# Kernel tuning notes

Hardware: AMD Instinct MI355X
Metric: run time of the kernel (lower is better)

Reference implementation:

```python
import jax, jax.numpy as jnp
import numpy as np

L2_LAMDA = 0.001
RECONS_LAMDA = 0.2
LB_TH = 0.01
B, N, D = 32, 2048, 256


def setup_inputs() -> dict:
    key = jax.random.key(0)
    k1, k2, k3, k4 = jax.random.split(key, 4)
    cur = jax.random.normal(k1, (B, N, D), jnp.float32)
    pre = jax.random.normal(k2, (B, N, D), jnp.float32)
    lim_r = float(np.sqrt(6.0 / (D + D)))  # xavier_uniform bound
    r_proj = jax.random.uniform(k3, (D, D), jnp.float32, -lim_r, lim_r)
    lim_i = float(np.sqrt(6.0 / (N + N)))
    incidence_m = jax.random.uniform(k4, (N, N), jnp.float32, -lim_i, lim_i)
    return {"cur": cur, "pre": pre, "r_proj": r_proj, "incidence_m": incidence_m}


def reference(cur, pre, r_proj, incidence_m):
    # torch forward detaches cur/pre
    cur = jax.lax.stop_gradient(cur)
    pre = jax.lax.stop_gradient(pre)
    # clamp(min=lb_th) then zero where not (> lb_th)  ==  keep original where > lb_th else 0
    W = jnp.where(incidence_m > LB_TH, incidence_m, 0.0)          # (N, N)
    proj = jnp.einsum('bnd,de->bne', cur, r_proj)                 # (B, N, D)
    neigh = jnp.einsum('nm,bmd->bnd', W, pre)                     # (B, N, D)
    recon_err = jnp.sqrt(jnp.sum((proj - neigh) ** 2, axis=-1))   # (B, N)
    # torch: max(sum(abs(row[None,:]), dim=0)) == max-abs of the masked row
    l1 = jnp.max(jnp.abs(W), axis=1)                              # (N,)
    l2 = jnp.sqrt(jnp.sum(W ** 2, axis=1))                        # (N,)
    per_node = recon_err * RECONS_LAMDA + l1[None, :] + L2_LAMDA * l2[None, :]
    loss = jnp.sum(per_node, axis=1, keepdims=True)               # (B, 1)
    return loss, incidence_m
```

## Files before the change

### kernel.cpp

```cpp
#include <hip/hip_runtime.h>


typedef __attribute__((ext_vector_type(8))) short bf16x8;
typedef __attribute__((ext_vector_type(8))) unsigned short ushort8;
typedef __attribute__((ext_vector_type(16))) float f32x16;

__device__ __forceinline__ unsigned short f2bf(float f) {
    union { float f; unsigned u; } x; x.f = f;
    unsigned r = x.u + 0x7fffu + ((x.u >> 16) & 1u);
    return (unsigned short)(r >> 16);
}

#define GLL16(g, l)                                                         \
    __builtin_amdgcn_global_load_lds(                                       \
        (const __attribute__((address_space(1))) void*)(g),                 \
        (__attribute__((address_space(3))) void*)(l), 16, 0, 0)

__device__ __forceinline__ void transpose_64x64(
    const float* __restrict__ src, unsigned short* __restrict__ dst,
    int R, int C, int r0, int c0, unsigned short* __restrict__ tile) {
    const int t = threadIdx.x;
    const int fr = t >> 4, fc = (t & 15) * 4;
#pragma unroll
    for (int it = 0; it < 4; ++it) {
        int m = fr + it * 16;
        float4 v = *(const float4*)(src + (size_t)(r0 + m) * C + c0 + fc);
        tile[(fc + 0) * 68 + m] = f2bf(v.x);
        tile[(fc + 1) * 68 + m] = f2bf(v.y);
        tile[(fc + 2) * 68 + m] = f2bf(v.z);
        tile[(fc + 3) * 68 + m] = f2bf(v.w);
    }
    __syncthreads();
    const int d = t >> 2, m0 = (t & 3) * 16;
    unsigned short v[16];
#pragma unroll
    for (int j = 0; j < 4; ++j)
        *(ushort4*)(v + j * 4) = *(const ushort4*)(tile + d * 68 + m0 + j * 4);
    unsigned short* dp = dst + (size_t)(c0 + d) * R + r0 + m0;
    ushort8 p0, p1;
#pragma unroll
    for (int j = 0; j < 8; ++j) { p0[j] = v[j]; p1[j] = v[8 + j]; }
    *(ushort8*)(dp) = p0;
    *(ushort8*)(dp + 8) = p1;
}

__global__ __launch_bounds__(256) void prep_inc(
    const float* __restrict__ inc, float* __restrict__ out_inc,
    unsigned short* __restrict__ Wneg, float* __restrict__ crow) {
    __shared__ float smax[4], ssum[4];
    const int row = blockIdx.x;
    const int t = threadIdx.x;
    const float4* src = (const float4*)(inc + (size_t)row * 2048);
    float4* dst = (float4*)(out_inc + (size_t)row * 2048);
    ushort4* wp = (ushort4*)(Wneg + (size_t)row * 2048);
    float lmax = 0.f, ss = 0.f;
#pragma unroll
    for (int it = 0; it < 2; ++it) {
        int i = it * 256 + t;
        float4 v = src[i];
        dst[i] = v;
        float w0 = v.x > 0.01f ? v.x : 0.f;
        float w1 = v.y > 0.01f ? v.y : 0.f;
        float w2 = v.z > 0.01f ? v.z : 0.f;
        float w3 = v.w > 0.01f ? v.w : 0.f;
        ushort4 p;
        p.x = f2bf(-w0); p.y = f2bf(-w1); p.z = f2bf(-w2); p.w = f2bf(-w3);
        wp[i] = p;
        lmax = fmaxf(lmax, fmaxf(fmaxf(w0, w1), fmaxf(w2, w3)));
        ss += w0 * w0 + w1 * w1 + w2 * w2 + w3 * w3;
    }
#pragma unroll
    for (int off = 32; off; off >>= 1) {
        lmax = fmaxf(lmax, __shfl_down(lmax, off));
        ss += __shfl_down(ss, off);
    }
    int wv = t >> 6, ln = t & 63;
    if (ln == 0) { smax[wv] = lmax; ssum[wv] = ss; }
    __syncthreads();
    if (t == 0) {
        float m = fmaxf(fmaxf(smax[0], smax[1]), fmaxf(smax[2], smax[3]));
        float s = ssum[0] + ssum[1] + ssum[2] + ssum[3];
        crow[row] = m + 0.001f * sqrtf(s);
    }
}

__global__ __launch_bounds__(256) void prep_tr(
    const float* __restrict__ pre, unsigned short* __restrict__ preT,
    const float* __restrict__ r_proj, unsigned short* __restrict__ rprojT,
    const float* __restrict__ cur, unsigned short* __restrict__ curbf) {
    __shared__ unsigned short tile[64 * 68];
    const int bid = blockIdx.x;
    const int t = threadIdx.x;
    if (bid < 4096) {
        const int b = bid >> 7;
        const int mt = (bid & 127) >> 2;
        const int dt = bid & 3;
        transpose_64x64(pre + (size_t)b * 524288, preT + (size_t)b * 524288,
                        2048, 256, mt * 64, dt * 64, tile);
    } else if (bid < 4112) {
        const int tt = bid - 4096;
        transpose_64x64(r_proj, rprojT, 256, 256, (tt >> 2) * 64, (tt & 3) * 64,
                        tile);
    } else {
        const size_t base = (size_t)(bid - 4112) * 8192;
#pragma unroll
        for (int i = 0; i < 8; ++i) {
            size_t idx = base + (size_t)(i * 256 + t) * 4;
            float4 v = *(const float4*)(cur + idx);
            ushort4 p;
            p.x = f2bf(v.x); p.y = f2bf(v.y); p.z = f2bf(v.z); p.w = f2bf(v.w);
            *(ushort4*)(curbf + idx) = p;
        }
    }
}

__global__ __launch_bounds__(1024) void gemm_diff(
    const unsigned short* __restrict__ Wneg,
    const unsigned short* __restrict__ curbf,
    const unsigned short* __restrict__ preT,
    const unsigned short* __restrict__ rprojT,
    float* __restrict__ Ssq)
{
    const int n0 = blockIdx.x * 256;
    const int b  = blockIdx.y;

    __shared__ unsigned short Ab[4 * 256 * 32];
    __shared__ unsigned short Bb[4 * 256 * 32];
    __shared__ float ssq[256];

    const int tid  = threadIdx.x;
    const int w    = tid >> 6;
    const int lane = tid & 63;
    const int l32  = lane & 31;
    const int half = lane >> 5;
    const int wm   = w >> 2;
    const int wn   = w & 3;
    const int w16  = w * 16;
    const int srow  = lane >> 2;
    const int sbyte = ((lane & 3) ^ ((lane >> 3) & 3)) * 16;
    const int q2    = (l32 >> 1) & 3;

    if (tid < 256) ssq[tid] = 0.f;

    f32x16 acc[2][2] = {};

    const unsigned short* curA = curbf + (size_t)b * 2048 * 256 + (size_t)n0 * 256;
    const unsigned short* preB = preT + (size_t)b * 256 * 2048;
    const unsigned short* An   = Wneg + (size_t)n0 * 2048;

#define STAGEPAIR(T, AB, AS, BB, BS, KK)                                       \
    {                                                                          \
        GLL16((const char*)((AB) + (size_t)(w16 + srow) * (AS) + (KK)) + sbyte,\
              (char*)Ab + ((T) & 3) * 16384 + w * 1024);                       \
        GLL16((const char*)((BB) + (size_t)(w16 + srow) * (BS) + (KK)) + sbyte,\
              (char*)Bb + ((T) & 3) * 16384 + w * 1024);                       \
    }

    STAGEPAIR(0, An, 2048, preB, 2048, 0);
    STAGEPAIR(1, An, 2048, preB, 2048, 32);
    STAGEPAIR(2, An, 2048, preB, 2048, 64);

    for (int t = 0; t < 72; ++t) {
        if (t < 70)      asm volatile("s_waitcnt vmcnt(4)" ::: "memory");
        else if (t == 70) asm volatile("s_waitcnt vmcnt(2)" ::: "memory");
        else              asm volatile("s_waitcnt vmcnt(0)" ::: "memory");
        asm volatile("s_barrier" ::: "memory");

        if (t < 69) {
            const int t3 = t + 3;
            const unsigned short *aB, *bB;
            int aS, bS, kk;
            if (t3 < 64) { aB = An;   aS = 2048; bB = preB;   bS = 2048; kk = t3 * 32; }
            else         { aB = curA; aS = 256;  bB = rprojT; bS = 256;  kk = (t3 - 64) * 32; }
            STAGEPAIR(t3, aB, aS, bB, bS, kk);
        }

        const unsigned short* Ac = Ab + (t & 3) * 8192;
        const unsigned short* Bc = Bb + (t & 3) * 8192;
#pragma unroll
        for (int ks = 0; ks < 2; ++ks) {
            const int co = (((ks << 1) + half) ^ q2) << 3;
            bf16x8 af[2], bfr[2];
#pragma unroll
            for (int mi = 0; mi < 2; ++mi)
                af[mi] = *(const bf16x8*)(Ac + (wm * 64 + mi * 32 + l32) * 32 + co);
#pragma unroll
            for (int ni = 0; ni < 2; ++ni)
                bfr[ni] = *(const bf16x8*)(Bc + (wn * 64 + ni * 32 + l32) * 32 + co);
#pragma unroll
            for (int mi = 0; mi < 2; ++mi)
#pragma unroll
                for (int ni = 0; ni < 2; ++ni)
                    acc[mi][ni] = __builtin_amdgcn_mfma_f32_32x32x16_bf16(
                        af[mi], bfr[ni], acc[mi][ni], 0, 0, 0);
        }
    }
    __syncthreads();

#pragma unroll
    for (int mi = 0; mi < 2; ++mi)
#pragma unroll
        for (int reg = 0; reg < 16; ++reg) {
            float s = 0.f;
#pragma unroll
            for (int ni = 0; ni < 2; ++ni) {
                float v = acc[mi][ni][reg];
                s += v * v;
            }
            s += __shfl_xor(s, 1);
            s += __shfl_xor(s, 2);
            s += __shfl_xor(s, 4);
            s += __shfl_xor(s, 8);
            s += __shfl_xor(s, 16);
            if (l32 == 0) {
                const int row = wm * 64 + mi * 32 +
                                (reg & 3) + 8 * (reg >> 2) + 4 * half;
                atomicAdd(&ssq[row], s);
            }
        }
    __syncthreads();
    if (tid < 256)
        Ssq[(size_t)b * 2048 + n0 + tid] = sqrtf(ssq[tid]);
}

__global__ void finalize(const float* __restrict__ Ssq,
                         const float* __restrict__ crow,
                         float* __restrict__ out) {
    const int b = blockIdx.x;
    float s1 = 0.f, s2 = 0.f;
    for (int i = threadIdx.x; i < 2048; i += 256) {
        s1 += Ssq[(size_t)b * 2048 + i];
        s2 += crow[i];
    }
#pragma unroll
    for (int off = 32; off; off >>= 1) {
        s1 += __shfl_down(s1, off);
        s2 += __shfl_down(s2, off);
    }
    __shared__ float sm1[4], sm2[4];
    int wv = threadIdx.x >> 6, ln = threadIdx.x & 63;
    if (ln == 0) { sm1[wv] = s1; sm2[wv] = s2; }
    __syncthreads();
    if (threadIdx.x == 0)
        out[b] = 0.2f * (sm1[0] + sm1[1] + sm1[2] + sm1[3])
               + (sm2[0] + sm2[1] + sm2[2] + sm2[3]);
}

extern "C" void kernel_launch(void* const* d_in, const int* in_sizes, int n_in,
                              void* d_out, int out_size, void* d_ws, size_t ws_size,
                              hipStream_t stream) {
    const float* cur    = (const float*)d_in[0];
    const float* pre    = (const float*)d_in[1];
    const float* r_proj = (const float*)d_in[2];
    const float* inc    = (const float*)d_in[3];
    float* out = (float*)d_out;

    char* ws = (char*)d_ws;
    unsigned short* Wneg   = (unsigned short*)(ws + 0);
    unsigned short* preT   = (unsigned short*)(ws + 8388608);
    unsigned short* rprojT = (unsigned short*)(ws + 41943040);
    float*          Sbuf   = (float*)(ws + 42074112);
    float*          crow   = (float*)(ws + 42336256);
    unsigned short* curbf  = (unsigned short*)(ws + 42344448);

    prep_inc<<<2048, 256, 0, stream>>>(inc, out + 32, Wneg, crow);
    prep_tr<<<6160, 256, 0, stream>>>(pre, preT, r_proj, rprojT, cur, curbf);
    gemm_diff<<<dim3(8, 32), 1024, 0, stream>>>(Wneg, curbf, preT, rprojT, Sbuf);
    finalize<<<32, 256, 0, stream>>>(Sbuf, crow, out);
}
```

Baseline: 265.6 us.

## Merge prep kernels, fold finalize into GEMM epilogue, remap blocks per XCD

Combines the incidence preprocessing and the transpose/convert kernels into one launch. The final per-batch reduction moves into the GEMM epilogue, which accumulates into the output with atomics after the output is zeroed in the prep kernel. This drops two kernel launches and the intermediate Ssq buffer. The GEMM grid is also remapped so each XCD handles whole batches, aiming to improve L2 reuse of the shared B operand. The trade-off is that atomic float accumulation makes the summation order nondeterministic.

```diff
diff --git a/kernel.cpp b/kernel.cpp
--- a/kernel.cpp
+++ b/kernel.cpp
@@ -44,65 +44,66 @@
     *(ushort8*)(dp + 8) = p1;
 }
 
-__global__ __launch_bounds__(256) void prep_inc(
+__global__ __launch_bounds__(256) void prep_all(
     const float* __restrict__ inc, float* __restrict__ out_inc,
-    unsigned short* __restrict__ Wneg, float* __restrict__ crow) {
-    __shared__ float smax[4], ssum[4];
-    const int row = blockIdx.x;
-    const int t = threadIdx.x;
-    const float4* src = (const float4*)(inc + (size_t)row * 2048);
-    float4* dst = (float4*)(out_inc + (size_t)row * 2048);
-    ushort4* wp = (ushort4*)(Wneg + (size_t)row * 2048);
-    float lmax = 0.f, ss = 0.f;
-#pragma unroll
-    for (int it = 0; it < 2; ++it) {
-        int i = it * 256 + t;
-        float4 v = src[i];
-        dst[i] = v;
-        float w0 = v.x > 0.01f ? v.x : 0.f;
-        float w1 = v.y > 0.01f ? v.y : 0.f;
-        float w2 = v.z > 0.01f ? v.z : 0.f;
-        float w3 = v.w > 0.01f ? v.w : 0.f;
-        ushort4 p;
-        p.x = f2bf(-w0); p.y = f2bf(-w1); p.z = f2bf(-w2); p.w = f2bf(-w3);
-        wp[i] = p;
-        lmax = fmaxf(lmax, fmaxf(fmaxf(w0, w1), fmaxf(w2, w3)));
-        ss += w0 * w0 + w1 * w1 + w2 * w2 + w3 * w3;
-    }
-#pragma unroll
-    for (int off = 32; off; off >>= 1) {
-        lmax = fmaxf(lmax, __shfl_down(lmax, off));
-        ss += __shfl_down(ss, off);
-    }
-    int wv = t >> 6, ln = t & 63;
-    if (ln == 0) { smax[wv] = lmax; ssum[wv] = ss; }
-    __syncthreads();
-    if (t == 0) {
-        float m = fmaxf(fmaxf(smax[0], smax[1]), fmaxf(smax[2], smax[3]));
-        float s = ssum[0] + ssum[1] + ssum[2] + ssum[3];
-        crow[row] = m + 0.001f * sqrtf(s);
-    }
-}
-
-__global__ __launch_bounds__(256) void prep_tr(
+    unsigned short* __restrict__ Wneg, float* __restrict__ crow,
     const float* __restrict__ pre, unsigned short* __restrict__ preT,
     const float* __restrict__ r_proj, unsigned short* __restrict__ rprojT,
-    const float* __restrict__ cur, unsigned short* __restrict__ curbf) {
+    const float* __restrict__ cur, unsigned short* __restrict__ curbf,
+    float* __restrict__ out_loss) {
     __shared__ unsigned short tile[64 * 68];
+    __shared__ float smax[4], ssum[4];
     const int bid = blockIdx.x;
     const int t = threadIdx.x;
-    if (bid < 4096) {
-        const int b = bid >> 7;
-        const int mt = (bid & 127) >> 2;
-        const int dt = bid & 3;
+
+    if (bid < 2048) {
+        if (bid == 0 && t < 32) out_loss[t] = 0.f;
+        const int row = bid;
+        const float4* src = (const float4*)(inc + (size_t)row * 2048);
+        float4* dst = (float4*)(out_inc + (size_t)row * 2048);
+        ushort4* wp = (ushort4*)(Wneg + (size_t)row * 2048);
+        float lmax = 0.f, ss = 0.f;
+#pragma unroll
+        for (int it = 0; it < 2; ++it) {
+            int i = it * 256 + t;
+            float4 v = src[i];
+            dst[i] = v;
+            float w0 = v.x > 0.01f ? v.x : 0.f;
+            float w1 = v.y > 0.01f ? v.y : 0.f;
+            float w2 = v.z > 0.01f ? v.z : 0.f;
+            float w3 = v.w > 0.01f ? v.w : 0.f;
+            ushort4 p;
+            p.x = f2bf(-w0); p.y = f2bf(-w1); p.z = f2bf(-w2); p.w = f2bf(-w3);
+            wp[i] = p;
+            lmax = fmaxf(lmax, fmaxf(fmaxf(w0, w1), fmaxf(w2, w3)));
+            ss += w0 * w0 + w1 * w1 + w2 * w2 + w3 * w3;
+        }
+#pragma unroll
+        for (int off = 32; off; off >>= 1) {
+            lmax = fmaxf(lmax, __shfl_down(lmax, off));
+            ss += __shfl_down(ss, off);
+        }
+        int wv = t >> 6, ln = t & 63;
+        if (ln == 0) { smax[wv] = lmax; ssum[wv] = ss; }
+        __syncthreads();
+        if (t == 0) {
+            float m = fmaxf(fmaxf(smax[0], smax[1]), fmaxf(smax[2], smax[3]));
+            float s = ssum[0] + ssum[1] + ssum[2] + ssum[3];
+            crow[row] = m + 0.001f * sqrtf(s);
+        }
+    } else if (bid < 6144) {
+        const int tt = bid - 2048;
+        const int b = tt >> 7;
+        const int mt = (tt & 127) >> 2;
+        const int dt = tt & 3;
         transpose_64x64(pre + (size_t)b * 524288, preT + (size_t)b * 524288,
                         2048, 256, mt * 64, dt * 64, tile);
-    } else if (bid < 4112) {
-        const int tt = bid - 4096;
+    } else if (bid < 6160) {
+        const int tt = bid - 6144;
         transpose_64x64(r_proj, rprojT, 256, 256, (tt >> 2) * 64, (tt & 3) * 64,
                         tile);
     } else {
-        const size_t base = (size_t)(bid - 4112) * 8192;
+        const size_t base = (size_t)(bid - 6160) * 8192;
 #pragma unroll
         for (int i = 0; i < 8; ++i) {
             size_t idx = base + (size_t)(i * 256 + t) * 4;
@@ -119,14 +120,19 @@
     const unsigned short* __restrict__ curbf,
     const unsigned short* __restrict__ preT,
     const unsigned short* __restrict__ rprojT,
-    float* __restrict__ Ssq)
+    const float* __restrict__ crow,
+    float* __restrict__ out_loss)
 {
-    const int n0 = blockIdx.x * 256;
-    const int b  = blockIdx.y;
+    const int i    = blockIdx.x;
+    const int xcd  = i & 7;
+    const int slot = i >> 3;
+    const int n0   = (slot & 7) * 256;
+    const int b    = xcd + ((slot >> 3) << 3);
 
     __shared__ unsigned short Ab[4 * 256 * 32];
     __shared__ unsigned short Bb[4 * 256 * 32];
     __shared__ float ssq[256];
+    __shared__ float red[16];
 
     const int tid  = threadIdx.x;
     const int w    = tid >> 6;
@@ -161,7 +167,7 @@
     STAGEPAIR(2, An, 2048, preB, 2048, 64);
 
     for (int t = 0; t < 72; ++t) {
-        if (t < 70)      asm volatile("s_waitcnt vmcnt(4)" ::: "memory");
+        if (t < 70)       asm volatile("s_waitcnt vmcnt(4)" ::: "memory");
         else if (t == 70) asm volatile("s_waitcnt vmcnt(2)" ::: "memory");
         else              asm volatile("s_waitcnt vmcnt(0)" ::: "memory");
         asm volatile("s_barrier" ::: "memory");
@@ -219,31 +225,19 @@
             }
         }
     __syncthreads();
-    if (tid < 256)
-        Ssq[(size_t)b * 2048 + n0 + tid] = sqrtf(ssq[tid]);
-}
-
-__global__ void finalize(const float* __restrict__ Ssq,
-                         const float* __restrict__ crow,
-                         float* __restrict__ out) {
-    const int b = blockIdx.x;
-    float s1 = 0.f, s2 = 0.f;
-    for (int i = threadIdx.x; i < 2048; i += 256) {
-        s1 += Ssq[(size_t)b * 2048 + i];
-        s2 += crow[i];
-    }
-#pragma unroll
-    for (int off = 32; off; off >>= 1) {
-        s1 += __shfl_down(s1, off);
-        s2 += __shfl_down(s2, off);
-    }
-    __shared__ float sm1[4], sm2[4];
-    int wv = threadIdx.x >> 6, ln = threadIdx.x & 63;
-    if (ln == 0) { sm1[wv] = s1; sm2[wv] = s2; }
-    __syncthreads();
-    if (threadIdx.x == 0)
-        out[b] = 0.2f * (sm1[0] + sm1[1] + sm1[2] + sm1[3])
-               + (sm2[0] + sm2[1] + sm2[2] + sm2[3]);
+
+    float contrib = 0.f;
+    if (tid < 256) contrib = 0.2f * sqrtf(ssq[tid]) + crow[n0 + tid];
+#pragma unroll
+    for (int off = 32; off; off >>= 1) contrib += __shfl_down(contrib, off);
+    if (lane == 0) red[w] = contrib;
+    __syncthreads();
+    if (tid == 0) {
+        float s = 0.f;
+#pragma unroll
+        for (int k = 0; k < 16; ++k) s += red[k];
+        atomicAdd(out_loss + b, s);
+    }
 }
 
 extern "C" void kernel_launch(void* const* d_in, const int* in_sizes, int n_in,
@@ -259,12 +253,11 @@
     unsigned short* Wneg   = (unsigned short*)(ws + 0);
     unsigned short* preT   = (unsigned short*)(ws + 8388608);
     unsigned short* rprojT = (unsigned short*)(ws + 41943040);
-    float*          Sbuf   = (float*)(ws + 42074112);
     float*          crow   = (float*)(ws + 42336256);
     unsigned short* curbf  = (unsigned short*)(ws + 42344448);
 
-    prep_inc<<<2048, 256, 0, stream>>>(inc, out + 32, Wneg, crow);
-    prep_tr<<<6160, 256, 0, stream>>>(pre, preT, r_proj, rprojT, cur, curbf);
-    gemm_diff<<<dim3(8, 32), 1024, 0, stream>>>(Wneg, curbf, preT, rprojT, Sbuf);
-    finalize<<<32, 256, 0, stream>>>(Sbuf, crow, out);
-}
+    prep_all<<<8208, 256, 0, stream>>>(inc, out + 32, Wneg, crow,
+                                       pre, preT, r_proj, rprojT,
+                                       cur, curbf, out);
+    gemm_diff<<<256, 1024, 0, stream>>>(Wneg, curbf, preT, rprojT, crow, out);
+}
```

Result: faster. 258.2 us (-2.8%).
